# Performance work log

Hardware: AMD Instinct MI355X
Metric: run time of the kernel (lower is better)

## Reference

```python
import jax, jax.numpy as jnp
import numpy as np

N_NODES = 1048576
N_SEG = 16384
NODES_PER_SEG = N_NODES // N_SEG
D = 128
EPS = 1e-5


def setup_inputs() -> dict:
    key = jax.random.key(0)
    ks = jax.random.split(key, 8)
    feat = jax.random.normal(ks[0], (N_NODES, D), dtype=jnp.float32)
    position_weight = jax.random.uniform(ks[1], (N_NODES,), dtype=jnp.float32)
    # equal-size segments (sessions): contiguous, sorted segment ids
    segment_ids = jnp.repeat(jnp.arange(N_SEG, dtype=jnp.int32), NODES_PER_SEG)
    # last node of each segment
    last_nodes = jnp.arange(N_SEG, dtype=jnp.int32) * NODES_PER_SEG + (NODES_PER_SEG - 1)
    # parameters
    gamma = jnp.ones((D,), dtype=jnp.float32)
    beta = jnp.zeros((D,), dtype=jnp.float32)
    s = 1.0 / np.sqrt(D)
    W_u = jax.random.uniform(ks[2], (D, D), dtype=jnp.float32, minval=-s, maxval=s)
    W_i = jax.random.uniform(ks[3], (D, D), dtype=jnp.float32, minval=-s, maxval=s)
    b_i = jax.random.uniform(ks[4], (D,), dtype=jnp.float32, minval=-s, maxval=s)
    w_e = jax.random.uniform(ks[5], (D,), dtype=jnp.float32, minval=-s, maxval=s)
    return {
        "feat": feat, "position_weight": position_weight,
        "last_nodes": last_nodes, "segment_ids": segment_ids,
        "gamma": gamma, "beta": beta, "W_u": W_u, "W_i": W_i,
        "b_i": b_i, "w_e": w_e, "num_segments": N_SEG,
    }


def reference(feat, position_weight, last_nodes, segment_ids, gamma, beta,
              W_u, W_i, b_i, w_e, num_segments):
    # BatchNorm1d (training-mode batch statistics)
    mean = feat.mean(axis=0)
    var = jnp.mean((feat - mean) ** 2, axis=0)
    f = (feat - mean) * (gamma / jnp.sqrt(var + EPS)) + beta  # [N, D]

    feat_u = f @ W_u.T                                         # [N, H]
    feat_last = f[last_nodes] @ W_i.T + b_i                    # [B, H]
    # broadcast_nodes: gather per-graph vector back to its nodes
    e = jax.nn.sigmoid(feat_u + feat_last[segment_ids]) @ w_e  # [N]

    # segment softmax over nodes of each graph
    m = jax.ops.segment_max(e, segment_ids, num_segments=num_segments)
    ex = jnp.exp(e - m[segment_ids])
    denom = jax.ops.segment_sum(ex, segment_ids, num_segments=num_segments)
    alpha = ex / denom[segment_ids]                            # [N]

    rst = jax.ops.segment_sum(f * alpha[:, None], segment_ids,
                              num_segments=num_segments)       # [B, D]
    position_rst = jax.ops.segment_sum(f * position_weight[:, None], segment_ids,
                                       num_segments=num_segments)  # [B, D]
    return rst, position_rst
```

## Files before the change

kernel.cpp:

```cpp
#include <hip/hip_runtime.h>

#define N_NODES 1048576
#define N_SEG   16384
#define NPS     64
#define D       128
#define EPS     1e-5f

typedef float f4 __attribute__((ext_vector_type(4)));
typedef float f32x4 __attribute__((ext_vector_type(4)));
typedef __bf16 bf16x8 __attribute__((ext_vector_type(8)));

__global__ __launch_bounds__(256) void k_stats(const float* __restrict__ feat,
                                               float* __restrict__ part) {
    int t = threadIdx.x;
    long gid = (long)blockIdx.x * 256 + t;
    const f4* f4p = (const f4*)feat;
    f4 s = {0.f,0.f,0.f,0.f}, q = {0.f,0.f,0.f,0.f};
#pragma unroll 8
    for (int k = 0; k < 64; ++k) {
        f4 v = f4p[gid + (long)k * 524288];
        s += v;
        q += v * v;
    }
    __shared__ f4 red[2][8][32];
    red[0][t >> 5][t & 31] = s;
    red[1][t >> 5][t & 31] = q;
    __syncthreads();
    int stat = t >> 7, c = t & 127;
    const float* base = (const float*)&red[stat][0][0];
    float acc = 0.f;
#pragma unroll
    for (int r = 0; r < 8; ++r) acc += base[r * 128 + c];
    part[(stat * 128 + c) * 2048 + blockIdx.x] = acc;
}

__global__ __launch_bounds__(256) void k_scale(const float* __restrict__ part,
                                               const float* __restrict__ gamma,
                                               const float* __restrict__ beta,
                                               float* __restrict__ scl,
                                               float* __restrict__ shf) {
    int t = threadIdx.x, c = blockIdx.x;
    float s1 = 0.f, s2 = 0.f;
#pragma unroll
    for (int j = 0; j < 8; ++j) {
        s1 += part[c * 2048 + t + 256 * j];
        s2 += part[(128 + c) * 2048 + t + 256 * j];
    }
    __shared__ float rs[256], rq[256];
    rs[t] = s1; rq[t] = s2;
    __syncthreads();
    for (int off = 128; off > 0; off >>= 1) {
        if (t < off) { rs[t] += rs[t + off]; rq[t] += rq[t + off]; }
        __syncthreads();
    }
    if (t == 0) {
        float mean = rs[0] / (float)N_NODES;
        float var  = rq[0] / (float)N_NODES - mean * mean;
        float sc   = gamma[c] * rsqrtf(var + EPS);
        scl[c] = sc;
        shf[c] = beta[c] - mean * sc;
    }
}

__global__ __launch_bounds__(256) void k_last(const float* __restrict__ feat,
                                              const int* __restrict__ last_nodes,
                                              const float* __restrict__ Wi,
                                              const float* __restrict__ bi,
                                              const float* __restrict__ scl,
                                              const float* __restrict__ shf,
                                              float* __restrict__ flp) {
    __shared__ float sWiT[128][129];
    __shared__ float fl[128];
    __shared__ float comb[128];
    int t = threadIdx.x;
    for (int i = t; i < 16384; i += 256) sWiT[i & 127][i >> 7] = Wi[i];
    __syncthreads();
    for (int s = 0; s < 32; ++s) {
        int seg = blockIdx.x * 32 + s;
        int row = last_nodes[seg];
        if (t < 128) fl[t] = feat[(long)row * 128 + t] * scl[t] + shf[t];
        __syncthreads();
        int h = t & 127, half = t >> 7;
        float acc = 0.f;
#pragma unroll 8
        for (int d = 64 * half; d < 64 * half + 64; ++d) acc += fl[d] * sWiT[d][h];
        if (half) comb[h] = acc;
        __syncthreads();
        if (!half) flp[seg * 128 + h] = acc + comb[h] + bi[h];
        __syncthreads();
    }
}

__device__ inline unsigned pk2(float x, float y) {
    unsigned a = __builtin_bit_cast(unsigned, x);
    unsigned b = __builtin_bit_cast(unsigned, y);
    a = (a + 0x7fffu + ((a >> 16) & 1u)) >> 16;
    b = (b + 0x7fffu + ((b >> 16) & 1u)) & 0xffff0000u;
    return a | b;
}
__device__ inline bf16x8 lds8(const unsigned short* p, int row, int kb) {
    int addr = (row * 256 + kb) ^ ((row & 7) << 4);
    return *(const bf16x8*)((const char*)p + addr);
}

__global__ __launch_bounds__(256, 2) void k_main(const float* __restrict__ feat,
                                                 const float* __restrict__ pw,
                                                 const float* __restrict__ Wu,
                                                 const float* __restrict__ we,
                                                 const float* __restrict__ scl,
                                                 const float* __restrict__ shf,
                                                 const float* __restrict__ flp,
                                                 float* __restrict__ out) {
    __shared__ __align__(16) unsigned short sWu[128 * 128];
    __shared__ __align__(16) unsigned short sA[64 * 128];
    __shared__ float epart[4][64];
    __shared__ float alpha[64];
    __shared__ __align__(16) float partR[8][128];
    __shared__ __align__(16) float partP[8][128];

    int t = threadIdx.x;
    int lane = t & 63, w = t >> 6;
    int c0 = 4 * (t & 31);
    f4 vscl = *(const f4*)(scl + c0);
    f4 vshf = *(const f4*)(shf + c0);

    const f4* Wu4 = (const f4*)Wu;
#pragma unroll
    for (int k = 0; k < 16; ++k) {
        int g = t + 256 * k;
        f4 v = Wu4[g];
        int h = g >> 5;
        int addr = (h * 256 + (g & 31) * 8) ^ ((h & 7) << 4);
        *(uint2*)((char*)sWu + addr) = make_uint2(pk2(v.x, v.y), pk2(v.z, v.w));
    }
    int h_a = (lane & 15) + 32 * w;
    int h_b = h_a + 16;
    float we0 = we[h_a], we1 = we[h_b];
    __syncthreads();

    for (int it = 0; it < 8; ++it) {
        int seg = blockIdx.x * 8 + it;
        const f4* src = (const f4*)(feat + (long)seg * NPS * D);
        f4 f[8];
        float pwv[8];
#pragma unroll
        for (int k = 0; k < 8; ++k) {
            f4 v = src[t + 256 * k];
            f[k] = v * vscl + vshf;
        }
#pragma unroll
        for (int k = 0; k < 8; ++k) pwv[k] = pw[seg * NPS + (t >> 5) + 8 * k];
        float fl0 = flp[seg * 128 + h_a];
        float fl1 = flp[seg * 128 + h_b];
#pragma unroll
        for (int k = 0; k < 8; ++k) {
            int n = (t >> 5) + 8 * k;
            int addr = (n * 256 + 8 * (t & 31)) ^ ((n & 7) << 4);
            *(uint2*)((char*)sA + addr) = make_uint2(pk2(f[k].x, f[k].y), pk2(f[k].z, f[k].w));
        }
        __syncthreads();

        f32x4 acc[4][2];
#pragma unroll
        for (int nf = 0; nf < 4; ++nf)
#pragma unroll
            for (int hf = 0; hf < 2; ++hf) acc[nf][hf] = (f32x4){0.f,0.f,0.f,0.f};
        int lo = lane & 15, g4 = lane >> 4;
#pragma unroll
        for (int kk = 0; kk < 4; ++kk) {
            int kb = kk * 64 + g4 * 16;
            bf16x8 b0 = lds8(sWu, h_a, kb);
            bf16x8 b1 = lds8(sWu, h_b, kb);
            bf16x8 a[4];
#pragma unroll
            for (int nf = 0; nf < 4; ++nf) a[nf] = lds8(sA, lo + 16 * nf, kb);
#pragma unroll
            for (int nf = 0; nf < 4; ++nf) {
                acc[nf][0] = __builtin_amdgcn_mfma_f32_16x16x32_bf16(a[nf], b0, acc[nf][0], 0, 0, 0);
                acc[nf][1] = __builtin_amdgcn_mfma_f32_16x16x32_bf16(a[nf], b1, acc[nf][1], 0, 0, 0);
            }
        }

#pragma unroll
        for (int nf = 0; nf < 4; ++nf) {
#pragma unroll
            for (int r = 0; r < 4; ++r) {
                float x0 = acc[nf][0][r] + fl0;
                float x1 = acc[nf][1][r] + fl1;
                float p = we0 / (1.f + __expf(-x0)) + we1 / (1.f + __expf(-x1));
                p += __shfl_xor(p, 1);
                p += __shfl_xor(p, 2);
                p += __shfl_xor(p, 4);
                p += __shfl_xor(p, 8);
                if ((lane & 15) == 0) epart[w][16 * nf + 4 * g4 + r] = p;
            }
        }
        __syncthreads();

        if (t < 64) {
            float e = epart[0][t] + epart[1][t] + epart[2][t] + epart[3][t];
            float m = e;
#pragma unroll
            for (int off = 32; off > 0; off >>= 1) m = fmaxf(m, __shfl_xor(m, off));
            float ex = __expf(e - m);
            float sd = ex;
#pragma unroll
            for (int off = 32; off > 0; off >>= 1) sd += __shfl_xor(sd, off);
            alpha[t] = ex / sd;
        }
        __syncthreads();

        f4 racc = {0.f,0.f,0.f,0.f}, pacc = {0.f,0.f,0.f,0.f};
#pragma unroll
        for (int k = 0; k < 8; ++k) {
            float av = alpha[(t >> 5) + 8 * k];
            racc += av * f[k];
            pacc += pwv[k] * f[k];
        }
        *(f4*)&partR[t >> 5][c0] = racc;
        *(f4*)&partP[t >> 5][c0] = pacc;
        __syncthreads();

        if (t < 128) {
            float s = 0.f;
#pragma unroll
            for (int r = 0; r < 8; ++r) s += partR[r][t];
            out[(long)seg * 128 + t] = s;
        } else {
            int c = t - 128;
            float s = 0.f;
#pragma unroll
            for (int r = 0; r < 8; ++r) s += partP[r][c];
            out[(long)N_SEG * 128 + (long)seg * 128 + c] = s;
        }
        __syncthreads();
    }
}

extern "C" void kernel_launch(void* const* d_in, const int* in_sizes, int n_in,
                              void* d_out, int out_size, void* d_ws, size_t ws_size,
                              hipStream_t stream) {
    const float* feat       = (const float*)d_in[0];
    const float* pw         = (const float*)d_in[1];
    const int*   last_nodes = (const int*)d_in[2];
    const float* gamma      = (const float*)d_in[4];
    const float* beta       = (const float*)d_in[5];
    const float* Wu         = (const float*)d_in[6];
    const float* Wi         = (const float*)d_in[7];
    const float* bi         = (const float*)d_in[8];
    const float* we         = (const float*)d_in[9];
    float* out = (float*)d_out;

    float* ws   = (float*)d_ws;
    float* part = ws;
    float* wscl = ws + 524288;
    float* wshf = ws + 524288 + 128;
    float* flp  = ws + 524288 + 256;

    k_stats<<<dim3(2048), dim3(256), 0, stream>>>(feat, part);
    k_scale<<<dim3(128),  dim3(256), 0, stream>>>(part, gamma, beta, wscl, wshf);
    k_last <<<dim3(512),  dim3(256), 0, stream>>>(feat, last_nodes, Wi, bi, wscl, wshf, flp);
    k_main <<<dim3(2048), dim3(256), 0, stream>>>(feat, pw, Wu, we, wscl, wshf, flp, out);
}
```

Before: 388.5 us.

## Prefetch next segment's features in k_main, alias reduction buffers, raise occupancy

The main kernel now loads the next segment's 64x128 feature tile into registers while it computes the current segment, so global-load latency overlaps with the MFMA and softmax work. The partial-sum reduction buffers now reuse the sA shared tile instead of their own arrays, which cuts LDS use, and launch bounds ask for 3 blocks per CU instead of 2. k_last is also reworked to handle two segments per pass, one per half-block, each with a full 128-term dot product. The prefetch doubles the feature registers held per thread, which may spill under the tighter register budget that 3 blocks per CU imposes.

```diff
diff --git a/kernel.cpp b/kernel.cpp
--- a/kernel.cpp
+++ b/kernel.cpp
@@ -70,23 +70,21 @@
                                               const float* __restrict__ shf,
                                               float* __restrict__ flp) {
     __shared__ float sWiT[128][129];
-    __shared__ float fl[128];
-    __shared__ float comb[128];
+    __shared__ float fl[2][128];
     int t = threadIdx.x;
     for (int i = t; i < 16384; i += 256) sWiT[i & 127][i >> 7] = Wi[i];
-    __syncthreads();
-    for (int s = 0; s < 32; ++s) {
-        int seg = blockIdx.x * 32 + s;
+    int half = t >> 7, c = t & 127;
+    float biv = bi[c];
+    __syncthreads();
+    for (int s = 0; s < 16; ++s) {
+        int seg = blockIdx.x * 32 + 2 * s + half;
         int row = last_nodes[seg];
-        if (t < 128) fl[t] = feat[(long)row * 128 + t] * scl[t] + shf[t];
-        __syncthreads();
-        int h = t & 127, half = t >> 7;
-        float acc = 0.f;
-#pragma unroll 8
-        for (int d = 64 * half; d < 64 * half + 64; ++d) acc += fl[d] * sWiT[d][h];
-        if (half) comb[h] = acc;
-        __syncthreads();
-        if (!half) flp[seg * 128 + h] = acc + comb[h] + bi[h];
+        fl[half][c] = feat[(long)row * 128 + c] * scl[c] + shf[c];
+        __syncthreads();
+        float acc = biv;
+#pragma unroll
+        for (int d = 0; d < 128; ++d) acc += fl[half][d] * sWiT[d][c];
+        flp[seg * 128 + c] = acc;
         __syncthreads();
     }
 }
@@ -103,7 +101,7 @@
     return *(const bf16x8*)((const char*)p + addr);
 }
 
-__global__ __launch_bounds__(256, 2) void k_main(const float* __restrict__ feat,
+__global__ __launch_bounds__(256, 3) void k_main(const float* __restrict__ feat,
                                                  const float* __restrict__ pw,
                                                  const float* __restrict__ Wu,
                                                  const float* __restrict__ we,
@@ -115,8 +113,8 @@
     __shared__ __align__(16) unsigned short sA[64 * 128];
     __shared__ float epart[4][64];
     __shared__ float alpha[64];
-    __shared__ __align__(16) float partR[8][128];
-    __shared__ __align__(16) float partP[8][128];
+    float* partR = (float*)sA;
+    float* partP = (float*)sA + 1024;
 
     int t = threadIdx.x;
     int lane = t & 63, w = t >> 6;
@@ -136,24 +134,33 @@
     int h_a = (lane & 15) + 32 * w;
     int h_b = h_a + 16;
     float we0 = we[h_a], we1 = we[h_b];
+
+    int seg0 = blockIdx.x * 8;
+    f4 f[8];
+    {
+        const f4* src = (const f4*)(feat + (long)seg0 * NPS * D);
+#pragma unroll
+        for (int k = 0; k < 8; ++k) f[k] = src[t + 256 * k];
+    }
     __syncthreads();
 
     for (int it = 0; it < 8; ++it) {
-        int seg = blockIdx.x * 8 + it;
-        const f4* src = (const f4*)(feat + (long)seg * NPS * D);
-        f4 f[8];
+        int seg = seg0 + it;
+        f4 fn[8];
+        if (it < 7) {
+            const f4* src = (const f4*)(feat + (long)(seg + 1) * NPS * D);
+#pragma unroll
+            for (int k = 0; k < 8; ++k) fn[k] = src[t + 256 * k];
+        }
         float pwv[8];
-#pragma unroll
-        for (int k = 0; k < 8; ++k) {
-            f4 v = src[t + 256 * k];
-            f[k] = v * vscl + vshf;
-        }
 #pragma unroll
         for (int k = 0; k < 8; ++k) pwv[k] = pw[seg * NPS + (t >> 5) + 8 * k];
         float fl0 = flp[seg * 128 + h_a];
         float fl1 = flp[seg * 128 + h_b];
+
 #pragma unroll
         for (int k = 0; k < 8; ++k) {
+            f[k] = f[k] * vscl + vshf;
             int n = (t >> 5) + 8 * k;
             int addr = (n * 256 + 8 * (t & 31)) ^ ((n & 7) << 4);
             *(uint2*)((char*)sA + addr) = make_uint2(pk2(f[k].x, f[k].y), pk2(f[k].z, f[k].w));
@@ -217,23 +224,28 @@
             racc += av * f[k];
             pacc += pwv[k] * f[k];
         }
-        *(f4*)&partR[t >> 5][c0] = racc;
-        *(f4*)&partP[t >> 5][c0] = pacc;
+        *(f4*)&partR[(t >> 5) * 128 + c0] = racc;
+        *(f4*)&partP[(t >> 5) * 128 + c0] = pacc;
         __syncthreads();
 
         if (t < 128) {
             float s = 0.f;
 #pragma unroll
-            for (int r = 0; r < 8; ++r) s += partR[r][t];
+            for (int r = 0; r < 8; ++r) s += partR[r * 128 + t];
             out[(long)seg * 128 + t] = s;
         } else {
             int c = t - 128;
             float s = 0.f;
 #pragma unroll
-            for (int r = 0; r < 8; ++r) s += partP[r][c];
+            for (int r = 0; r < 8; ++r) s += partP[r * 128 + c];
             out[(long)N_SEG * 128 + (long)seg * 128 + c] = s;
         }
         __syncthreads();
+
+        if (it < 7) {
+#pragma unroll
+            for (int k = 0; k < 8; ++k) f[k] = fn[k];
+        }
     }
 }
 
```

New measurement: 446.8 us. 15.0% more time.
